# Kernel optimization log

Hardware: AMD Instinct MI355X
Metric: run time of the kernel (lower is better)

Reference implementation:

```python
import jax, jax.numpy as jnp
import numpy as np

N, E, IN, HID, EE, L, NB = 20000, 256000, 64, 128, 32, 3, 8


def _silu(x):
    return x * jax.nn.sigmoid(x)


def setup_inputs() -> dict:
    key = jax.random.key(0)
    ks = list(jax.random.split(key, 32))

    def nrm(k, shape, fan_in):
        return jax.random.normal(k, shape, dtype=jnp.float32) / np.sqrt(fan_in)

    inp = {}
    inp["H_t"] = jax.random.normal(ks[0], (N, IN), dtype=jnp.float32)
    inp["X_t"] = jax.random.normal(ks[1], (N, 3), dtype=jnp.float32)
    inp["cond_embedding"] = jax.random.normal(ks[2], (N, HID), dtype=jnp.float32)
    inp["t"] = jax.random.uniform(ks[3], (N,), dtype=jnp.float32)
    inp["edges"] = jax.random.randint(ks[4], (2, E), 0, N)
    inp["edge_types"] = jax.random.randint(ks[5], (E,), 0, 2)
    inp["generate_mask"] = jax.random.bernoulli(ks[6], 0.7, (N,))
    inp["batch_ids"] = jnp.sort(jax.random.randint(ks[7], (N,), 0, NB))
    # input MLP: (IN + 2*HID) -> HID -> HID -> HID, 3 linear layers
    d0 = IN + 2 * HID
    inp["mlp_W0"] = nrm(ks[8], (d0, HID), d0)
    inp["mlp_b0"] = jnp.zeros((HID,), jnp.float32)
    inp["mlp_W1"] = nrm(ks[9], (HID, HID), HID)
    inp["mlp_b1"] = jnp.zeros((HID,), jnp.float32)
    inp["mlp_W2"] = nrm(ks[10], (HID, HID), HID)
    inp["mlp_b2"] = jnp.zeros((HID,), jnp.float32)
    inp["edge_table"] = jax.random.normal(ks[11], (2, EE), dtype=jnp.float32)
    # encoder (EGNN-style message passing), stacked over L layers
    de = 2 * HID + 1 + EE  # [h_src, h_dst, dist^2, edge_embed]
    inp["We"] = nrm(ks[12], (L, de, HID), de)
    inp["be"] = jnp.zeros((L, HID), jnp.float32)
    inp["Wx"] = nrm(ks[13], (L, HID, 1), HID)
    inp["bx"] = jnp.zeros((L, 1), jnp.float32)
    inp["Wh"] = nrm(ks[14], (L, 2 * HID, HID), 2 * HID)
    inp["bh"] = jnp.zeros((L, HID), jnp.float32)
    inp["h2i_W"] = nrm(ks[15], (HID, IN), HID)
    inp["h2i_b"] = jnp.zeros((IN,), jnp.float32)
    return inp


def reference(H_t, X_t, cond_embedding, t, mlp_W0, mlp_b0, mlp_W1, mlp_b1,
              mlp_W2, mlp_b2, edge_table, We, be, Wx, bx, Wh, bh,
              h2i_W, h2i_b, edges, edge_types, generate_mask, batch_ids):
    n = H_t.shape[0]
    hid = mlp_W2.shape[1]
    # sinusoidal time embedding (dim = hidden_size)
    half = hid // 2
    freqs = jnp.exp(jnp.arange(half, dtype=jnp.float32) * (-np.log(10000.0) / (half - 1)))
    ang = t[:, None] * freqs[None, :]
    t_embed = jnp.concatenate([jnp.sin(ang), jnp.cos(ang)], axis=-1)  # (N, hid)
    # input MLP
    feat = jnp.concatenate([H_t, cond_embedding, t_embed], axis=-1)
    h = jax.nn.relu(feat @ mlp_W0 + mlp_b0)
    h = jax.nn.relu(h @ mlp_W1 + mlp_b1)
    h = h @ mlp_W2 + mlp_b2
    eemb = edge_table[edge_types]  # (E, EE)
    src, dst = edges[0], edges[1]
    cnt = jax.ops.segment_sum(jnp.ones((src.shape[0], 1), h.dtype), dst, num_segments=n)
    x = X_t
    for l in range(We.shape[0]):
        diff = x[src] - x[dst]                              # (E, 3)
        d2 = jnp.sum(diff * diff, axis=-1, keepdims=True)   # (E, 1)
        m_in = jnp.concatenate([h[src], h[dst], d2, eemb], axis=-1)
        msg = _silu(m_in @ We[l] + be[l])                   # (E, hid)
        w = msg @ Wx[l] + bx[l]                             # (E, 1)
        agg_x = jax.ops.segment_sum(diff * w, dst, num_segments=n)
        x = x + agg_x / (cnt + 1.0)
        agg_m = jax.ops.segment_sum(msg, dst, num_segments=n)
        h = h + _silu(jnp.concatenate([h, agg_m], axis=-1) @ Wh[l] + bh[l])
    mask = generate_mask[:, None]
    v_X = jnp.where(mask, x, jnp.zeros_like(x))
    v_H = jnp.where(mask, h @ h2i_W + h2i_b, 0.0)
    return (v_H, v_X)
```

## Files before the change

### kernel.cpp

```cpp
#include <hip/hip_runtime.h>
#include <math.h>

#define NN 20000
#define NE 256000
#define IN_DIM 64
#define HID 128
#define DE 289
#define D0 320
#define TILE_E 64
#define NB64 313
#define NUB 8
#define SRCMASK 0x3FFFFFFF

typedef unsigned short u16;
typedef unsigned int u32;
typedef unsigned long long u64;
typedef __attribute__((ext_vector_type(8))) short short8;
typedef __attribute__((ext_vector_type(4))) float float4v;

#define OFF_WE   0
#define OFF_W0   122880
#define OFF_W1   163840
#define OFF_W2   180224
#define OFF_WH   196608
#define OFF_H2I  294912
#define PACK_TOT 303104

static __device__ __forceinline__ u16 f2bf(float f) {
    unsigned int u = __float_as_uint(f);
    u += 0x7fffu + ((u >> 16) & 1u);
    return (u16)(u >> 16);
}
static __device__ __forceinline__ float bf2f(u16 s) {
    return __uint_as_float(((unsigned int)s) << 16);
}
static __device__ __forceinline__ float bflo(u32 u) { return bf2f((u16)(u & 0xffffu)); }
static __device__ __forceinline__ float bfhi(u32 u) { return bf2f((u16)(u >> 16)); }
static __device__ __forceinline__ u32 pack2(float a, float b) {
    return (u32)f2bf(a) | ((u32)f2bf(b) << 16);
}
static __device__ __forceinline__ uint4 pack8(const float* v) {
    uint4 r;
    r.x = (u32)f2bf(v[0]) | ((u32)f2bf(v[1]) << 16);
    r.y = (u32)f2bf(v[2]) | ((u32)f2bf(v[3]) << 16);
    r.z = (u32)f2bf(v[4]) | ((u32)f2bf(v[5]) << 16);
    r.w = (u32)f2bf(v[6]) | ((u32)f2bf(v[7]) << 16);
    return r;
}
static __device__ __forceinline__ float silu(float v) {
    return v * (1.f / (1.f + __expf(-v)));
}

__global__ __launch_bounds__(256) void hist_kernel(
    const float* __restrict__ X_t, const int* __restrict__ edges,
    float* __restrict__ x, int* __restrict__ deg)
{
    int gid = blockIdx.x * blockDim.x + threadIdx.x;
    int stride = gridDim.x * blockDim.x;
    for (int i = gid; i < NN * 3; i += stride) x[i] = X_t[i];
    for (int e = gid; e < NE; e += stride)
        atomicAdd(&deg[edges[NE + e]], 1);
}

__global__ __launch_bounds__(1024) void scan_kernel(
    const int* __restrict__ deg, int* __restrict__ row_start, int* __restrict__ head)
{
    __shared__ int s[1024];
    int tx = threadIdx.x;
    const int per = (NN + 1023) / 1024;
    int st = tx * per, en = st + per;
    if (st > NN) st = NN;
    if (en > NN) en = NN;
    int sum = 0;
    for (int i = st; i < en; ++i) sum += deg[i];
    s[tx] = sum;
    __syncthreads();
    for (int off = 1; off < 1024; off <<= 1) {
        int t = (tx >= off) ? s[tx - off] : 0;
        __syncthreads();
        s[tx] += t;
        __syncthreads();
    }
    int run = (tx == 0) ? 0 : s[tx - 1];
    for (int i = st; i < en; ++i) {
        row_start[i] = run; head[i] = run; run += deg[i];
    }
    if (tx == 1023) row_start[NN] = run;
}

__global__ __launch_bounds__(256) void scatter_kernel(
    const int* __restrict__ edges, const int* __restrict__ etype,
    int* __restrict__ head,
    int* __restrict__ src_s)
{
    int gid = blockIdx.x * blockDim.x + threadIdx.x;
    int stride = gridDim.x * blockDim.x;
    for (int e = gid; e < NE; e += stride) {
        int d = edges[NE + e];
        int p = atomicAdd(&head[d], 1);
        src_s[p] = edges[e] | (etype[e] << 30);
    }
}

__global__ __launch_bounds__(256) void pack_all_kernel(
    const float* __restrict__ We, const float* __restrict__ W0,
    const float* __restrict__ W1, const float* __restrict__ W2,
    const float* __restrict__ Wh, const float* __restrict__ h2i,
    u16* __restrict__ Bp)
{
    int idx = blockIdx.x * 256 + threadIdx.x;
    if (idx >= PACK_TOT) return;
    const float* src; int N = 128, Ksrc; int r;
    if (idx < OFF_W0) {
        int layer = idx / 40960; r = idx - layer * 40960;
        src = We + (size_t)layer * DE * HID; Ksrc = DE;
    } else if (idx < OFF_W1) { r = idx - OFF_W0; src = W0; Ksrc = 320; }
    else if (idx < OFF_W2)   { r = idx - OFF_W1; src = W1; Ksrc = 128; }
    else if (idx < OFF_WH)   { r = idx - OFF_W2; src = W2; Ksrc = 128; }
    else if (idx < OFF_H2I) {
        int t = idx - OFF_WH; int layer = t / 32768; r = t - layer * 32768;
        src = Wh + (size_t)layer * 256 * HID; Ksrc = 256;
    } else { r = idx - OFF_H2I; src = h2i; Ksrc = 128; N = 64; }
    int ntc = N / 16;
    int j = r & 7, lane = (r >> 3) & 63;
    int rem = r >> 9;
    int nt = rem % ntc, ks = rem / ntc;
    int k = ks * 32 + ((lane >> 4) << 3) + j;
    int c = nt * 16 + (lane & 15);
    Bp[idx] = f2bf((k < Ksrc) ? src[(size_t)k * N + c] : 0.f);
}

__global__ __launch_bounds__(256) void precomp_tv_kernel(
    const float* __restrict__ edge_table, const float* __restrict__ We,
    const float* __restrict__ be, float* __restrict__ tv, float* __restrict__ wed2)
{
    int idx = blockIdx.x * 256 + threadIdx.x;
    if (idx < 768) {
        int f = idx & 127, t = (idx >> 7) & 1, l = idx >> 8;
        float acc = be[l * 128 + f];
        const float* W = We + (size_t)l * DE * HID;
        #pragma unroll
        for (int k = 0; k < 32; ++k)
            acc += edge_table[t * 32 + k] * W[(size_t)(257 + k) * HID + f];
        tv[l * 256 + t * 128 + f] = acc;
    } else if (idx < 1152) {
        int r = idx - 768;
        int f = r & 127, l = r >> 7;
        wed2[l * 128 + f] = We[(size_t)l * DE * HID + (size_t)256 * HID + f];
    }
}

__global__ __launch_bounds__(256) void node_mlp_mfma_kernel(
    const float* __restrict__ H_t, const float* __restrict__ cond,
    const float* __restrict__ t_in,
    const u16* __restrict__ W0p, const float* __restrict__ b0,
    const u16* __restrict__ W1p, const float* __restrict__ b1,
    const u16* __restrict__ W2p, const float* __restrict__ b2,
    const u16* __restrict__ WEp, u16* __restrict__ Cbf,
    float* __restrict__ h, u16* __restrict__ h_bf)
{
    __shared__ u16 s_A[64 * 64];
    __shared__ u16 s_B[64 * 128];
    __shared__ u16 s_h[64 * 128];
    __shared__ float s_t[64];

    int tx = threadIdx.x;
    int n0 = blockIdx.x * 64;
    int l = tx & 63, w = tx >> 6;
    int mt_base = (w & 1) * 2, nt_base = (w >> 1) * 4;
    const float cfr = -logf(10000.f) / 63.f;

    if (tx < 64) s_t[tx] = (n0 + tx < NN) ? t_in[n0 + tx] : 0.f;

    float4v acc[2][4];
    #pragma unroll
    for (int mi = 0; mi < 2; ++mi)
        #pragma unroll
        for (int ni = 0; ni < 4; ++ni) acc[mi][ni] = (float4v){0.f,0.f,0.f,0.f};

    for (int t = 0; t < 5; ++t) {
        __syncthreads();
        #pragma unroll
        for (int it = 0; it < 2; ++it) {
            int flat = it * 256 + tx;
            int n = flat >> 3, sl = flat & 7;
            int c = sl ^ (n & 7);
            int k0 = t * 64 + c * 8;
            float tv8[8];
            int gn = n0 + n;
            if (gn < NN) {
                if (k0 < 192) {
                    const float* src = (k0 < 64) ? &H_t[(size_t)gn * IN_DIM + k0]
                                                 : &cond[(size_t)gn * HID + (k0 - 64)];
                    float4 a = *(const float4*)src;
                    float4 b = *(const float4*)(src + 4);
                    tv8[0]=a.x; tv8[1]=a.y; tv8[2]=a.z; tv8[3]=a.w;
                    tv8[4]=b.x; tv8[5]=b.y; tv8[6]=b.z; tv8[7]=b.w;
                } else {
                    float tv = s_t[n];
                    int jj = (k0 - 192) & 63;
                    bool is_sin = (k0 < 256);
                    #pragma unroll
                    for (int jx = 0; jx < 8; ++jx) {
                        float ang = tv * __expf(cfr * (float)(jj + jx));
                        tv8[jx] = is_sin ? __sinf(ang) : __cosf(ang);
                    }
                }
            } else {
                #pragma unroll
                for (int jx = 0; jx < 8; ++jx) tv8[jx] = 0.f;
            }
            *(uint4*)&s_A[n * 64 + sl * 8] = pack8(tv8);
        }
        #pragma unroll
        for (int it = 0; it < 4; ++it) {
            int flat = it * 256 + tx;
            ((uint4*)s_B)[flat] = ((const uint4*)(W0p + (size_t)t * 8192))[flat];
        }
        __syncthreads();
        #pragma unroll
        for (int s = 0; s < 2; ++s) {
            short8 af[2], bfv[4];
            #pragma unroll
            for (int mi = 0; mi < 2; ++mi) {
                int m = (mt_base + mi) * 16 + (l & 15);
                int c = s * 4 + (l >> 4);
                int slot = c ^ (l & 7);
                af[mi] = *(const short8*)(s_A + m * 64 + slot * 8);
            }
            #pragma unroll
            for (int ni = 0; ni < 4; ++ni)
                bfv[ni] = *(const short8*)(s_B + ((s * 8 + nt_base + ni) * 64 + l) * 8);
            #pragma unroll
            for (int mi = 0; mi < 2; ++mi)
                #pragma unroll
                for (int ni = 0; ni < 4; ++ni)
                    acc[mi][ni] = __builtin_amdgcn_mfma_f32_16x16x32_bf16(
                        af[mi], bfv[ni], acc[mi][ni], 0, 0, 0);
        }
    }
    #pragma unroll
    for (int mi = 0; mi < 2; ++mi) {
        #pragma unroll
        for (int ni = 0; ni < 4; ++ni) {
            int f = (nt_base + ni) * 16 + (l & 15);
            float bv = b0[f];
            #pragma unroll
            for (int r = 0; r < 4; ++r) {
                int m = (mt_base + mi) * 16 + (l >> 4) * 4 + r;
                float v = fmaxf(acc[mi][ni][r] + bv, 0.f);
                int slot = (f >> 3) ^ (m & 7);
                s_h[m * 128 + slot * 8 + (f & 7)] = f2bf(v);
            }
            acc[mi][ni] = (float4v){0.f,0.f,0.f,0.f};
        }
    }
    for (int t = 0; t < 2; ++t) {
        __syncthreads();
        #pragma unroll
        for (int it = 0; it < 4; ++it) {
            int flat = it * 256 + tx;
            ((uint4*)s_B)[flat] = ((const uint4*)(W1p + (size_t)t * 8192))[flat];
        }
        __syncthreads();
        #pragma unroll
        for (int s = 0; s < 2; ++s) {
            short8 af[2], bfv[4];
            #pragma unroll
            for (int mi = 0; mi < 2; ++mi) {
                int m = (mt_base + mi) * 16 + (l & 15);
                int c = t * 8 + s * 4 + (l >> 4);
                int slot = c ^ (l & 7);
                af[mi] = *(const short8*)(s_h + m * 128 + slot * 8);
            }
            #pragma unroll
            for (int ni = 0; ni < 4; ++ni)
                bfv[ni] = *(const short8*)(s_B + ((s * 8 + nt_base + ni) * 64 + l) * 8);
            #pragma unroll
            for (int mi = 0; mi < 2; ++mi)
                #pragma unroll
                for (int ni = 0; ni < 4; ++ni)
                    acc[mi][ni] = __builtin_amdgcn_mfma_f32_16x16x32_bf16(
                        af[mi], bfv[ni], acc[mi][ni], 0, 0, 0);
        }
    }
    __syncthreads();
    #pragma unroll
// ... 23 lines not shown
        #pragma unroll
        for (int s = 0; s < 2; ++s) {
            short8 af[2], bfv[4];
            #pragma unroll
            for (int mi = 0; mi < 2; ++mi) {
                int m = (mt_base + mi) * 16 + (l & 15);
                int c = t * 8 + s * 4 + (l >> 4);
                int slot = c ^ (l & 7);
                af[mi] = *(const short8*)(s_h + m * 128 + slot * 8);
            }
            #pragma unroll
            for (int ni = 0; ni < 4; ++ni)
                bfv[ni] = *(const short8*)(s_B + ((s * 8 + nt_base + ni) * 64 + l) * 8);
            #pragma unroll
            for (int mi = 0; mi < 2; ++mi)
                #pragma unroll
                for (int ni = 0; ni < 4; ++ni)
                    acc[mi][ni] = __builtin_amdgcn_mfma_f32_16x16x32_bf16(
                        af[mi], bfv[ni], acc[mi][ni], 0, 0, 0);
        }
    }
    __syncthreads();
    #pragma unroll
    for (int mi = 0; mi < 2; ++mi) {
        #pragma unroll
        for (int ni = 0; ni < 4; ++ni) {
            int f = (nt_base + ni) * 16 + (l & 15);
            float bv = b2[f];
            #pragma unroll
            for (int r = 0; r < 4; ++r) {
                int m = (mt_base + mi) * 16 + (l >> 4) * 4 + r;
                int gn = n0 + m;
                float v = acc[mi][ni][r] + bv;
                int slot = (f >> 3) ^ (m & 7);
                s_h[m * 128 + slot * 8 + (f & 7)] = f2bf(v);
                if (gn < NN) {
                    h[(size_t)gn * HID + f] = v;
                    h_bf[(size_t)gn * HID + f] = f2bf(v);
                }
            }
        }
    }

    for (int sd = 0; sd < 2; ++sd) {
        #pragma unroll
        for (int mi = 0; mi < 2; ++mi)
            #pragma unroll
            for (int ni = 0; ni < 4; ++ni) acc[mi][ni] = (float4v){0.f,0.f,0.f,0.f};
        #pragma unroll
        for (int th = 0; th < 2; ++th) {
            int t = sd * 2 + th;
            __syncthreads();
            #pragma unroll
            for (int it = 0; it < 4; ++it) {
                int flat = it * 256 + tx;
                ((uint4*)s_B)[flat] = ((const uint4*)(WEp + (size_t)t * 8192))[flat];
            }
            __syncthreads();
            #pragma unroll
            for (int s = 0; s < 2; ++s) {
                short8 af[2], bfv[4];
                #pragma unroll
                for (int mi = 0; mi < 2; ++mi) {
                    int m = (mt_base + mi) * 16 + (l & 15);
                    int c = th * 8 + s * 4 + (l >> 4);
                    int slot = c ^ (l & 7);
                    af[mi] = *(const short8*)(s_h + m * 128 + slot * 8);
                }
                #pragma unroll
                for (int ni = 0; ni < 4; ++ni)
                    bfv[ni] = *(const short8*)(s_B + ((s * 8 + nt_base + ni) * 64 + l) * 8);
                #pragma unroll
                for (int mi = 0; mi < 2; ++mi)
                    #pragma unroll
                    for (int ni = 0; ni < 4; ++ni)
                        acc[mi][ni] = __builtin_amdgcn_mfma_f32_16x16x32_bf16(
                            af[mi], bfv[ni], acc[mi][ni], 0, 0, 0);
            }
        }
        #pragma unroll
        for (int mi = 0; mi < 2; ++mi) {
            #pragma unroll
            for (int ni = 0; ni < 4; ++ni) {
                int f = sd * 128 + (nt_base + ni) * 16 + (l & 15);
                #pragma unroll
                for (int r = 0; r < 4; ++r) {
                    int m = (mt_base + mi) * 16 + (l >> 4) * 4 + r;
                    int gn = n0 + m;
                    if (gn < NN)
                        Cbf[(size_t)gn * 256 + f] = f2bf(acc[mi][ni][r]);
                }
            }
        }
    }
}

__global__ __launch_bounds__(256) void cvec_kernel(
    const u16* __restrict__ h_bf, const u16* __restrict__ WEp,
    u16* __restrict__ Cbf)
{
    __shared__ u16 s_A[64 * 64];
    __shared__ u16 s_B[64 * 128];

    int tx = threadIdx.x;
    int n0 = blockIdx.x * 64;
    int l = tx & 63, w = tx >> 6;
    int mt_base = (w & 1) * 2, nt_base = (w >> 1) * 4;

    float4v acc[2][2][4];
    #pragma unroll
    for (int sd = 0; sd < 2; ++sd)
        #pragma unroll
        for (int mi = 0; mi < 2; ++mi)
            #pragma unroll
            for (int ni = 0; ni < 4; ++ni)
                acc[sd][mi][ni] = (float4v){0.f,0.f,0.f,0.f};

    for (int t = 0; t < 4; ++t) {
        __syncthreads();
        #pragma unroll
        for (int it = 0; it < 2; ++it) {
            int flat = it * 256 + tx;
            int n = flat >> 3, sl = flat & 7;
            int c = sl ^ (n & 7);
            int gn = n0 + n;
            uint4 v = make_uint4(0,0,0,0);
            if (gn < NN) v = *(const uint4*)(h_bf + (size_t)gn * 128 + (t & 1) * 64 + c * 8);
            *(uint4*)&s_A[n * 64 + sl * 8] = v;
        }
        #pragma unroll
        for (int it = 0; it < 4; ++it) {
            int flat = it * 256 + tx;
            ((uint4*)s_B)[flat] = ((const uint4*)(WEp + (size_t)t * 8192))[flat];
        }
        __syncthreads();
        int sd = t >> 1;
        #pragma unroll
        for (int s = 0; s < 2; ++s) {
            short8 af[2], bfv[4];
            #pragma unroll
            for (int mi = 0; mi < 2; ++mi) {
                int m = (mt_base + mi) * 16 + (l & 15);
                int c = s * 4 + (l >> 4);
                int slot = c ^ (l & 7);
                af[mi] = *(const short8*)(s_A + m * 64 + slot * 8);
            }
            #pragma unroll
            for (int ni = 0; ni < 4; ++ni)
                bfv[ni] = *(const short8*)(s_B + ((s * 8 + nt_base + ni) * 64 + l) * 8);
            #pragma unroll
            for (int mi = 0; mi < 2; ++mi)
                #pragma unroll
                for (int ni = 0; ni < 4; ++ni)
                    acc[sd][mi][ni] = __builtin_amdgcn_mfma_f32_16x16x32_bf16(
                        af[mi], bfv[ni], acc[sd][mi][ni], 0, 0, 0);
        }
    }
    #pragma unroll
    for (int sd = 0; sd < 2; ++sd) {
        #pragma unroll
        for (int mi = 0; mi < 2; ++mi) {
            #pragma unroll
            for (int ni = 0; ni < 4; ++ni) {
                int f = sd * 128 + (nt_base + ni) * 16 + (l & 15);
                #pragma unroll
                for (int r = 0; r < 4; ++r) {
                    int m = (mt_base + mi) * 16 + (l >> 4) * 4 + r;
                    int gn = n0 + m;
                    if (gn < NN)
                        Cbf[(size_t)gn * 256 + f] = f2bf(acc[sd][mi][ni][r]);
                }
            }
        }
    }
}

__global__ __launch_bounds__(512, 4) void node_fused_kernel(
    float* __restrict__ h, u16* __restrict__ h_bf,
    const float* __restrict__ x_in, float* __restrict__ x_out,
    const u16* __restrict__ Cbf,
    const int* __restrict__ src_s,
    const int* __restrict__ row_start,
    const float* __restrict__ tv_l, const float* __restrict__ wed2_l,
    const float* __restrict__ Wx_l, const float* __restrict__ bx_l,
    const u16* __restrict__ Whp_l, const float* __restrict__ bh_l)
{
    __shared__ u16 s_A[16 * 256];

    int tx = threadIdx.x;
    int n0 = blockIdx.x * NUB;
    int l = tx & 63, w = tx >> 6;
    int i = w;
    int gn = n0 + i;
    int p = l & 31, q = l >> 5;

    if (tx < 256) {
        int n = tx >> 4, c = tx & 15;
        int slot = c ^ (n & 7);
        uint4 v = make_uint4(0, 0, 0, 0);
        if (n < NUB) v = *(const uint4*)(h_bf + (size_t)(n0 + n) * 128 + c * 8);
        *(uint4*)&s_A[n * 256 + slot * 8] = v;
    } else if (tx < 384) {
        int n = 8 + ((tx - 256) >> 4), c = 16 + (tx & 15);
        int slot = c ^ (n & 7);
        *(uint4*)&s_A[n * 256 + slot * 8] = make_uint4(0, 0, 0, 0);
    }

    float c0[4], d01[4], wed[4], wx[4];
    {
        uint2 cd = *(const uint2*)(Cbf + (size_t)gn * 256 + 128 + p * 4);
        float cdv0 = bflo(cd.x), cdv1 = bfhi(cd.x), cdv2 = bflo(cd.y), cdv3 = bfhi(cd.y);
        float4 t0 = *(const float4*)(tv_l + p * 4);
        float4 t1 = *(const float4*)(tv_l + 128 + p * 4);
        float4 wd = *(const float4*)(wed2_l + p * 4);
        float4 wv = *(const float4*)(Wx_l + p * 4);
        c0[0] = t0.x + cdv0; c0[1] = t0.y + cdv1; c0[2] = t0.z + cdv2; c0[3] = t0.w + cdv3;
        d01[0] = t1.x - t0.x; d01[1] = t1.y - t0.y; d01[2] = t1.z - t0.z; d01[3] = t1.w - t0.w;
        wed[0] = wd.x; wed[1] = wd.y; wed[2] = wd.z; wed[3] = wd.w;
        wx[0] = wv.x; wx[1] = wv.y; wx[2] = wv.z; wx[3] = wv.w;
    }
    float bx32 = bx_l[0] * (1.f / 32.f);

    int rs = row_start[gn], re = row_start[gn + 1];
    int d = re - rs;

    float xd0 = x_in[gn * 3 + 0], xd1 = x_in[gn * 3 + 1], xd2 = x_in[gn * 3 + 2];

    float ag[4] = {0.f, 0.f, 0.f, 0.f};
    float sx = 0.f, sy = 0.f, sz = 0.f;

    for (int e0 = 0; e0 < d; e0 += 64) {
        int nchunk = d - e0; if (nchunk > 64) nchunk = 64;
        int sp_l = (l < nchunk) ? src_s[rs + e0 + l] : 0;
        float gx_l = 0.f, gy_l = 0.f, gz_l = 0.f, d2_l = 0.f;
        if (l < nchunk) {
            int sm = sp_l & SRCMASK;
            gx_l = x_in[sm * 3 + 0] - xd0;
            gy_l = x_in[sm * 3 + 1] - xd1;
            gz_l = x_in[sm * 3 + 2] - xd2;
            d2_l = gx_l * gx_l + gy_l * gy_l + gz_l * gz_l;
        }

        auto FETCH = [&](int lj, uint2& cc, float& et) {
            int spE = __shfl(sp_l, lj);
            cc = make_uint2(0u, 0u); et = 0.f;
            if (lj < nchunk) {
                cc = *(const uint2*)(Cbf + (size_t)(spE & SRCMASK) * 256 + p * 4);
                et = (float)((u32)spE >> 30);
            }
        };
        auto PROC = [&](int lj, uint2 cc, float ee) {
            float dxe = __shfl(gx_l, lj);
            float dye = __shfl(gy_l, lj);
            float dze = __shfl(gz_l, lj);
            float d2e = __shfl(d2_l, lj);
            float av[4];
            av[0] = bflo(cc.x); av[1] = bfhi(cc.x);
            av[2] = bflo(cc.y); av[3] = bfhi(cc.y);
            float wpart = bx32;
            #pragma unroll
            for (int f = 0; f < 4; ++f) {
                float t = __fmaf_rn(d2e, wed[f], c0[f]);
                t = __fmaf_rn(ee, d01[f], t);
                float v = av[f] + t;
                float m = silu(v);
                ag[f] += m;
                wpart = __fmaf_rn(m, wx[f], wpart);
            }
            sx = __fmaf_rn(dxe, wpart, sx);
            sy = __fmaf_rn(dye, wpart, sy);
            sz = __fmaf_rn(dze, wpart, sz);
        };

        int ljA = q, ljB = q + 2, ljC = q + 4, ljD = q + 6, ljn = q + 8;
        uint2 ccA, ccB, ccC, ccD; float etA, etB, etC, etD;
        FETCH(ljA, ccA, etA); FETCH(ljB, ccB, etB);
        FETCH(ljC, ccC, etC); FETCH(ljD, ccD, etD);
        while (ljA < nchunk) {
            PROC(ljA, ccA, etA); ljA = ljn; ljn += 2; FETCH(ljA, ccA, etA);
            if (ljB >= nchunk) break;
            PROC(ljB, ccB, etB); ljB = ljn; ljn += 2; FETCH(ljB, ccB, etB);
            if (ljC >= nchunk) break;
            PROC(ljC, ccC, etC); ljC = ljn; ljn += 2; FETCH(ljC, ccC, etC);
            if (ljD >= nchunk) break;
            PROC(ljD, ccD, etD); ljD = ljn; ljn += 2; FETCH(ljD, ccD, etD);
        }
    }

    #pragma unroll
    for (int f = 0; f < 4; ++f) ag[f] += __shfl_xor(ag[f], 32);
    #pragma unroll
    for (int off = 1; off <= 32; off <<= 1) {
        sx += __shfl_xor(sx, off);
        sy += __shfl_xor(sy, off);
        sz += __shfl_xor(sz, off);
    }
    if (l < 32) {
        int c2 = 16 + (p >> 1);
        int slot = c2 ^ (i & 7);
        uint2 o;
        o.x = pack2(ag[0], ag[1]);
        o.y = pack2(ag[2], ag[3]);
        *(uint2*)&s_A[i * 256 + slot * 8 + (p & 1) * 4] = o;
    }
    if (l == 0) {
        float inv = 1.f / ((float)d + 1.f);
        x_out[gn * 3 + 0] = xd0 + sx * inv;
        x_out[gn * 3 + 1] = xd1 + sy * inv;
        x_out[gn * 3 + 2] = xd2 + sz * inv;
    }

    __syncthreads();

    float4v acc = (float4v){0.f, 0.f, 0.f, 0.f};
    #pragma unroll
    for (int t = 0; t < 4; ++t) {
        #pragma unroll
        for (int s = 0; s < 2; ++s) {
            int m = l & 15;
            int c = t * 8 + s * 4 + (l >> 4);
            int slot = c ^ (l & 7);
            short8 af = *(const short8*)(s_A + m * 256 + slot * 8);
            short8 bfv = *(const short8*)(Whp_l + (size_t)t * 8192 + ((s * 8 + w) * 64 + l) * 8);
            acc = __builtin_amdgcn_mfma_f32_16x16x32_bf16(af, bfv, acc, 0, 0, 0);
        }
    }
    {
        int f = w * 16 + (l & 15);
        float bv = bh_l[f];
        #pragma unroll
        for (int r = 0; r < 4; ++r) {
            int m = (l >> 4) * 4 + r;
            if (m < NUB) {
                int gn2 = n0 + m;
                float v = acc[r] + bv;
                float hn = h[(size_t)gn2 * HID + f] + silu(v);
                h[(size_t)gn2 * HID + f] = hn;
                h_bf[(size_t)gn2 * HID + f] = f2bf(hn);
            }
        }
    }
}

__global__ __launch_bounds__(256) void final_mfma_kernel(
    const u16* __restrict__ h_bf, const float* __restrict__ x,
    const int* __restrict__ gmask,
    const u16* __restrict__ h2ip, const float* __restrict__ b,
    float* __restrict__ out)
{
    __shared__ u16 s_A[64 * 128];
    __shared__ u16 s_B[4096];

    int tx = threadIdx.x;
    int n0 = blockIdx.x * 64;
    int l = tx & 63, w = tx >> 6;
    int mt_base = (w & 1) * 2, nt_base = (w >> 1) * 2;

    #pragma unroll
    for (int it = 0; it < 4; ++it) {
        int flat = it * 256 + tx;
        int n = flat >> 4, c = flat & 15;
        int slot = c ^ (n & 7);
        int gn = n0 + n;
        uint4 v = make_uint4(0,0,0,0);
        if (gn < NN) v = *(const uint4*)(h_bf + (size_t)gn * 128 + c * 8);
        *(uint4*)&s_A[n * 128 + slot * 8] = v;
    }

    float4v acc[2][2];
    #pragma unroll
    for (int mi = 0; mi < 2; ++mi)
        #pragma unroll
        for (int ni = 0; ni < 2; ++ni) acc[mi][ni] = (float4v){0.f,0.f,0.f,0.f};

    for (int t = 0; t < 2; ++t) {
        __syncthreads();
        #pragma unroll
        for (int it = 0; it < 2; ++it) {
            int flat = it * 256 + tx;
            ((uint4*)s_B)[flat] = ((const uint4*)(h2ip + (size_t)t * 4096))[flat];
        }
        __syncthreads();
        #pragma unroll
        for (int s = 0; s < 2; ++s) {
            short8 af[2], bfv[2];
            #pragma unroll
            for (int mi = 0; mi < 2; ++mi) {
                int m = (mt_base + mi) * 16 + (l & 15);
                int c = t * 8 + s * 4 + (l >> 4);
                int slot = c ^ (l & 7);
                af[mi] = *(const short8*)(s_A + m * 128 + slot * 8);
            }
            #pragma unroll
            for (int ni = 0; ni < 2; ++ni)
                bfv[ni] = *(const short8*)(s_B + ((s * 4 + nt_base + ni) * 64 + l) * 8);
            #pragma unroll
            for (int mi = 0; mi < 2; ++mi)
                #pragma unroll
                for (int ni = 0; ni < 2; ++ni)
                    acc[mi][ni] = __builtin_amdgcn_mfma_f32_16x16x32_bf16(
                        af[mi], bfv[ni], acc[mi][ni], 0, 0, 0);
        }
    }
    #pragma unroll
    for (int mi = 0; mi < 2; ++mi) {
        #pragma unroll
        for (int ni = 0; ni < 2; ++ni) {
            int f = (nt_base + ni) * 16 + (l & 15);
            float bv = b[f];
            #pragma unroll
            for (int r = 0; r < 4; ++r) {
                int m = (mt_base + mi) * 16 + (l >> 4) * 4 + r;
                int gn = n0 + m;
                if (gn < NN)
                    out[(size_t)gn * IN_DIM + f] = gmask[gn] ? (acc[mi][ni][r] + bv) : 0.f;
            }
        }
    }
    if (tx < 192) {
        int i = tx / 3, c = tx % 3;
        int gn = n0 + i;
// ... 255 lines not shown
        acc[4] += f1.x*w; acc[5] += f1.y*w; acc[6] += f1.z*w; acc[7] += f1.w*w;
        acc[8] += f2.x*w; acc[9] += f2.y*w; acc[10]+= f2.z*w; acc[11]+= f2.w*w;
        acc[12]+= f3.x*w; acc[13]+= f3.y*w; acc[14]+= f3.z*w; acc[15]+= f3.w*w;
    }
    #pragma unroll
    for (int i = 0; i < 16; ++i) {
        float v = acc[i];
        h[(n0 + i) * HID + tx] = s_in[tx][i] + silu(v);
    }
    if (tx < 48) {
        int i = tx / 3, c = tx % 3;
        int n = n0 + i;
        x[n * 3 + c] += agg_x[n * 3 + c] / (cnt[n] + 1.f);
    }
}

__global__ __launch_bounds__(64) void final_fb_kernel(
    const float* __restrict__ h, const float* __restrict__ x,
    const int* __restrict__ gmask,
    const float* __restrict__ W, const float* __restrict__ b,
    float* __restrict__ out)
{
    __shared__ float s_h[8][HID];
    int n0 = blockIdx.x * 8;
    int tx = threadIdx.x;
    for (int idx = tx; idx < 8 * HID; idx += 64) {
        int i = idx >> 7, k = idx & 127;
        s_h[i][k] = h[(n0 + i) * HID + k];
    }
    __syncthreads();
    float acc[8];
    float bv = b[tx];
    #pragma unroll
    for (int i = 0; i < 8; ++i) acc[i] = bv;
    for (int k = 0; k < HID; ++k) {
        float w = W[k * IN_DIM + tx];
        #pragma unroll
        for (int i = 0; i < 8; ++i) acc[i] += s_h[i][k] * w;
    }
    #pragma unroll
    for (int i = 0; i < 8; ++i) {
        int n = n0 + i;
        out[n * IN_DIM + tx] = gmask[n] ? acc[i] : 0.f;
    }
    if (tx < 24) {
        int i = tx / 3, c = tx % 3;
        int n = n0 + i;
        out[NN * IN_DIM + n * 3 + c] = gmask[n] ? x[n * 3 + c] : 0.f;
    }
}

extern "C" void kernel_launch(void* const* d_in, const int* in_sizes, int n_in,
                              void* d_out, int out_size, void* d_ws, size_t ws_size,
                              hipStream_t stream) {
    const float* H_t   = (const float*)d_in[0];
    const float* X_t   = (const float*)d_in[1];
    const float* cond  = (const float*)d_in[2];
    const float* t_in  = (const float*)d_in[3];
    const int*   edges = (const int*)d_in[4];
    const int*   etype = (const int*)d_in[5];
    const int*   gmask = (const int*)d_in[6];
    const float* W0 = (const float*)d_in[8];
    const float* b0 = (const float*)d_in[9];
    const float* W1 = (const float*)d_in[10];
    const float* b1 = (const float*)d_in[11];
    const float* W2 = (const float*)d_in[12];
    const float* b2 = (const float*)d_in[13];
    const float* edge_table = (const float*)d_in[14];
    const float* We = (const float*)d_in[15];
    const float* be = (const float*)d_in[16];
    const float* Wx = (const float*)d_in[17];
    const float* bx = (const float*)d_in[18];
    const float* Wh = (const float*)d_in[19];
    const float* bh = (const float*)d_in[20];
    const float* h2i_W = (const float*)d_in[21];
    const float* h2i_b = (const float*)d_in[22];

    char* p = (char*)d_ws;
    float* h = (float*)p;           p += (size_t)NN * HID * 4;
    u16* h_bf = (u16*)p;            p += (size_t)NN * HID * 2;
    float* xa = (float*)p;          p += (size_t)NN * 3 * 4;
    float* xb = (float*)p;          p += (size_t)NN * 3 * 4;
    u16* Cbf = (u16*)p;             p += (size_t)NN * 256 * 2;
    u16* Bpack = (u16*)p;           p += (size_t)PACK_TOT * 2;
    float* tv = (float*)p;          p += (size_t)768 * 4;
    float* wed2 = (float*)p;        p += (size_t)384 * 4;
    int* row_start = (int*)p;       p += (size_t)(NN + 4) * 4;
    int* deg = (int*)p;             p += (size_t)NN * 4;
    int* head = (int*)p;            p += (size_t)NN * 4;
    int* src_s = (int*)p;           p += (size_t)NE * 4;
    size_t need = (size_t)(p - (char*)d_ws);

    if (ws_size >= need) {
        hipMemsetAsync(deg, 0, NN * sizeof(int), stream);
        hist_kernel<<<256, 256, 0, stream>>>(X_t, edges, xa, deg);
        scan_kernel<<<1, 1024, 0, stream>>>(deg, row_start, head);
        scatter_kernel<<<256, 256, 0, stream>>>(edges, etype, head, src_s);
        pack_all_kernel<<<(PACK_TOT + 255) / 256, 256, 0, stream>>>(
            We, W0, W1, W2, Wh, h2i_W, Bpack);
        precomp_tv_kernel<<<5, 256, 0, stream>>>(edge_table, We, be, tv, wed2);
        node_mlp_mfma_kernel<<<NB64, 256, 0, stream>>>(
            H_t, cond, t_in,
            Bpack + OFF_W0, b0, Bpack + OFF_W1, b1, Bpack + OFF_W2, b2,
            Bpack + OFF_WE, Cbf,
            h, h_bf);
        for (int l = 0; l < 3; ++l) {
            if (l > 0)
                cvec_kernel<<<NB64, 256, 0, stream>>>(
                    h_bf, Bpack + OFF_WE + (size_t)l * 40960, Cbf);
            const float* xin = (l & 1) ? xb : xa;
            float* xout = (l & 1) ? xa : xb;
            node_fused_kernel<<<NN / NUB, 512, 0, stream>>>(
                h, h_bf, xin, xout, Cbf, src_s, row_start,
                tv + (size_t)l * 256, wed2 + (size_t)l * 128,
                Wx + l * HID, bx + l,
                Bpack + OFF_WH + (size_t)l * 32768, bh + l * HID);
        }
        final_mfma_kernel<<<NB64, 256, 0, stream>>>(
            h_bf, xb, gmask, Bpack + OFF_H2I, h2i_b, (float*)d_out);
    } else {
        float* ws    = (float*)d_ws;
        float* fh    = ws;
        float* fx    = fh + NN * HID;
        float* cnt   = fx + NN * 3;
        float* fagg_m = cnt + NN;
        float* fagg_x = fagg_m + NN * HID;

        hipMemsetAsync(cnt, 0, NN * sizeof(float), stream);
        init_fb_kernel<<<256, 256, 0, stream>>>(X_t, edges, fx, cnt);
        node_mlp_kernel<<<NN / 16, 128, 0, stream>>>(H_t, cond, t_in,
                                                     W0, b0, W1, b1, W2, b2, fh);
        for (int l = 0; l < 3; ++l) {
            hipMemsetAsync(fagg_m, 0, (size_t)NN * 131 * sizeof(float), stream);
            edge_gemm_fb_kernel<<<NE / TILE_E, 256, 0, stream>>>(
                fh, fx, edges, etype, edge_table,
                We + (size_t)l * DE * HID, be + l * HID,
                Wx + l * HID, bx + l, fagg_m, fagg_x);
            node_update_fb_kernel<<<NN / 16, 128, 0, stream>>>(
                fh, fx, fagg_m, fagg_x, cnt,
                Wh + (size_t)l * 256 * HID, bh + l * HID);
        }
        final_fb_kernel<<<NN / 8, 64, 0, stream>>>(fh, fx, gmask, h2i_W, h2i_b, (float*)d_out);
    }
}
```

Measured before the change: 372.0 us.

## Split edge aggregation from Wh update and fuse next-layer cvec into Wh kernel

Replaces the per-node fused kernel, where each wave handled one node's edges plus a tiny MFMA, with two kernels. The first is a wave-per-4-nodes edge aggregation kernel that walks a contiguous CSR edge range using readlane broadcasts and writes bf16 agg_m. The second is a 64-node-tile MFMA kernel that applies the Wh update and immediately computes the next layer's per-node We projections from shared memory, which removes the separate cvec launch. The edge-type constant is also folded into Cbf at write time. This trades an extra agg_bf round trip through global memory for better MFMA tiling and fewer launches, and the per-wave serial flush logic may cost latency.

```diff
diff --git a/kernel.cpp b/kernel.cpp
--- a/kernel.cpp
+++ b/kernel.cpp
@@ -9,7 +9,7 @@
 #define D0 320
 #define TILE_E 64
 #define NB64 313
-#define NUB 8
+#define NPW 4
 #define SRCMASK 0x3FFFFFFF
 
 typedef unsigned short u16;
@@ -49,6 +49,9 @@
 }
 static __device__ __forceinline__ float silu(float v) {
     return v * (1.f / (1.f + __expf(-v)));
+}
+static __device__ __forceinline__ float rdlane_f(float v, int j) {
+    return __int_as_float(__builtin_amdgcn_readlane(__float_as_int(v), j));
 }
 
 __global__ __launch_bounds__(256) void hist_kernel(
@@ -156,7 +159,8 @@
     const u16* __restrict__ W0p, const float* __restrict__ b0,
     const u16* __restrict__ W1p, const float* __restrict__ b1,
     const u16* __restrict__ W2p, const float* __restrict__ b2,
-    const u16* __restrict__ WEp, u16* __restrict__ Cbf,
+    const u16* __restrict__ WEp, const float* __restrict__ tv0,
+    u16* __restrict__ Cbf,
     float* __restrict__ h, u16* __restrict__ h_bf)
 {
     __shared__ u16 s_A[64 * 64];
@@ -197,12 +201,12 @@
                     tv8[0]=a.x; tv8[1]=a.y; tv8[2]=a.z; tv8[3]=a.w;
                     tv8[4]=b.x; tv8[5]=b.y; tv8[6]=b.z; tv8[7]=b.w;
                 } else {
-                    float tv = s_t[n];
+                    float tvv = s_t[n];
                     int jj = (k0 - 192) & 63;
                     bool is_sin = (k0 < 256);
                     #pragma unroll
                     for (int jx = 0; jx < 8; ++jx) {
-                        float ang = tv * __expf(cfr * (float)(jj + jx));
+                        float ang = tvv * __expf(cfr * (float)(jj + jx));
                         tv8[jx] = is_sin ? __sinf(ang) : __cosf(ang);
                     }
                 }
@@ -392,59 +396,182 @@
         for (int mi = 0; mi < 2; ++mi) {
             #pragma unroll
             for (int ni = 0; ni < 4; ++ni) {
-                int f = sd * 128 + (nt_base + ni) * 16 + (l & 15);
+                int fq = (nt_base + ni) * 16 + (l & 15);
+                int f = sd * 128 + fq;
+                float tadd = (sd == 1) ? tv0[fq] : 0.f;
                 #pragma unroll
                 for (int r = 0; r < 4; ++r) {
                     int m = (mt_base + mi) * 16 + (l >> 4) * 4 + r;
                     int gn = n0 + m;
                     if (gn < NN)
-                        Cbf[(size_t)gn * 256 + f] = f2bf(acc[mi][ni][r]);
+                        Cbf[(size_t)gn * 256 + f] = f2bf(acc[mi][ni][r] + tadd);
                 }
             }
         }
     }
 }
 
-__global__ __launch_bounds__(256) void cvec_kernel(
-    const u16* __restrict__ h_bf, const u16* __restrict__ WEp,
-    u16* __restrict__ Cbf)
+__global__ __launch_bounds__(256) void edge_agg_kernel(
+    const float* __restrict__ x_in, float* __restrict__ x_out,
+    const u16* __restrict__ Cbf, u16* __restrict__ agg_bf,
+    const int* __restrict__ src_s,
+    const int* __restrict__ row_start,
+    const float* __restrict__ tv_l, const float* __restrict__ wed2_l,
+    const float* __restrict__ Wx_l, const float* __restrict__ bx_l)
+{
+    int tx = threadIdx.x;
+    int l = tx & 63;
+    int wg = blockIdx.x * 4 + (tx >> 6);
+    int n0w = wg * NPW;
+
+    float2 wed = *(const float2*)(wed2_l + 2 * l);
+    float2 wxv = *(const float2*)(Wx_l + 2 * l);
+    float tva0 = tv_l[2 * l],       tva1 = tv_l[2 * l + 1];
+    float tvb0 = tv_l[128 + 2 * l], tvb1 = tv_l[128 + 2 * l + 1];
+    float d01_0 = tvb0 - tva0, d01_1 = tvb1 - tva1;
+    float bx64 = bx_l[0] * (1.f / 64.f);
+
+    int rsv = row_start[n0w + (l < NPW ? l : NPW)];
+    int rs0w = __builtin_amdgcn_readlane(rsv, 0);
+    int reN  = __builtin_amdgcn_readlane(rsv, NPW);
+    int b1 = __builtin_amdgcn_readlane(rsv, 1);
+    int b2 = __builtin_amdgcn_readlane(rsv, 2);
+    int b3 = __builtin_amdgcn_readlane(rsv, 3);
+
+    u32 cdA = *(const u32*)(Cbf + (size_t)(n0w + 0) * 256 + 128 + 2 * l);
+    u32 cdB = *(const u32*)(Cbf + (size_t)(n0w + 1) * 256 + 128 + 2 * l);
+    u32 cdC = *(const u32*)(Cbf + (size_t)(n0w + 2) * 256 + 128 + 2 * l);
+    u32 cdD = *(const u32*)(Cbf + (size_t)(n0w + 3) * 256 + 128 + 2 * l);
+
+    int cur = 0;
+    int nstart = rs0w;
+    int bnext = b1;
+    float c0f0 = bflo(cdA), c0f1 = bfhi(cdA);
+    float ag0 = 0.f, ag1 = 0.f, sx = 0.f, sy = 0.f, sz = 0.f;
+
+    auto FLUSH = [&]() {
+        float rx = sx, ry = sy, rz = sz;
+        #pragma unroll
+        for (int off = 1; off < 64; off <<= 1) {
+            rx += __shfl_xor(rx, off);
+            ry += __shfl_xor(ry, off);
+            rz += __shfl_xor(rz, off);
+        }
+        int gn = n0w + cur;
+        *(u32*)(agg_bf + (size_t)gn * 128 + 2 * l) = pack2(ag0, ag1);
+        if (l == 0) {
+            float inv = 1.f / ((float)(bnext - nstart) + 1.f);
+            x_out[gn * 3 + 0] = x_in[gn * 3 + 0] + rx * inv;
+            x_out[gn * 3 + 1] = x_in[gn * 3 + 1] + ry * inv;
+            x_out[gn * 3 + 2] = x_in[gn * 3 + 2] + rz * inv;
+        }
+        ag0 = 0.f; ag1 = 0.f; sx = 0.f; sy = 0.f; sz = 0.f;
+        nstart = bnext;
+        cur++;
+        cdA = cdB; cdB = cdC; cdC = cdD;
+        c0f0 = bflo(cdA); c0f1 = bfhi(cdA);
+        if (cur < NPW) bnext = __builtin_amdgcn_readlane(rsv, cur + 1);
+    };
+
+    const char* cb = (const char*)Cbf;
+    int lx4 = l << 2;
+
+    for (int base = rs0w; base < reN; base += 64) {
+        int nch = reN - base; if (nch > 64) nch = 64;
+        int voff_l = 0;
+        float et_l = 0.f, gx_l = 0.f, gy_l = 0.f, gz_l = 0.f, d2_l = 0.f;
+        if (l < nch) {
+            int pos_l = base + l;
+            int sp = src_s[pos_l];
+            int sm = sp & SRCMASK;
+            int k = (pos_l >= b1) + (pos_l >= b2) + (pos_l >= b3);
+            int dn = n0w + k;
+            voff_l = sm * 512;
+            et_l = (float)((u32)sp >> 30);
+            gx_l = x_in[sm * 3 + 0] - x_in[dn * 3 + 0];
+            gy_l = x_in[sm * 3 + 1] - x_in[dn * 3 + 1];
+            gz_l = x_in[sm * 3 + 2] - x_in[dn * 3 + 2];
+            d2_l = gx_l * gx_l + gy_l * gy_l + gz_l * gz_l;
+        }
+        auto LD = [&](int t) -> u32 {
+            int so = __builtin_amdgcn_readlane(voff_l, t & 63);
+            return *(const u32*)(cb + (u32)so + lx4);
+        };
+        auto BODY = [&](int j, u32 cc) {
+            int pos = base + j;
+            while (pos == bnext) FLUSH();
+            float s_et = rdlane_f(et_l, j);
+            float s_dx = rdlane_f(gx_l, j);
+            float s_dy = rdlane_f(gy_l, j);
+            float s_dz = rdlane_f(gz_l, j);
+            float s_d2 = rdlane_f(d2_l, j);
+            float av0 = bflo(cc), av1 = bfhi(cc);
+            float t0 = __fmaf_rn(s_d2, wed.x, c0f0);
+            t0 = __fmaf_rn(s_et, d01_0, t0) + av0;
+            float t1 = __fmaf_rn(s_d2, wed.y, c0f1);
+            t1 = __fmaf_rn(s_et, d01_1, t1) + av1;
+            float m0 = silu(t0), m1 = silu(t1);
+            ag0 += m0; ag1 += m1;
+            float wpart = __fmaf_rn(m1, wxv.y, __fmaf_rn(m0, wxv.x, bx64));
+            sx = __fmaf_rn(s_dx, wpart, sx);
+            sy = __fmaf_rn(s_dy, wpart, sy);
+            sz = __fmaf_rn(s_dz, wpart, sz);
+        };
+
+        u32 cA = LD(0), cB = LD(1), cC = LD(2), cD = LD(3);
+        int j = 0;
+        while (j < nch) {
+            BODY(j, cA); cA = LD(j + 4); if (++j >= nch) break;
+            BODY(j, cB); cB = LD(j + 4); if (++j >= nch) break;
+            BODY(j, cC); cC = LD(j + 4); if (++j >= nch) break;
+            BODY(j, cD); cD = LD(j + 4); ++j;
+        }
+    }
+    while (cur < NPW) FLUSH();
+}
+
+__global__ __launch_bounds__(256) void wh_cvec_kernel(
+    float* __restrict__ h, u16* __restrict__ h_bf,
+    const u16* __restrict__ agg_bf,
+    const u16* __restrict__ Whp_l, const float* __restrict__ bh_l,
+    const u16* __restrict__ WEp_next, const float* __restrict__ tv_next,
+    u16* __restrict__ Cbf, int do_cvec)
 {
     __shared__ u16 s_A[64 * 64];
     __shared__ u16 s_B[64 * 128];
+    __shared__ u16 s_h[64 * 128];
 
     int tx = threadIdx.x;
     int n0 = blockIdx.x * 64;
     int l = tx & 63, w = tx >> 6;
     int mt_base = (w & 1) * 2, nt_base = (w >> 1) * 4;
 
-    float4v acc[2][2][4];
-    #pragma unroll
-    for (int sd = 0; sd < 2; ++sd)
-        #pragma unroll
-        for (int mi = 0; mi < 2; ++mi)
-            #pragma unroll
-            for (int ni = 0; ni < 4; ++ni)
-                acc[sd][mi][ni] = (float4v){0.f,0.f,0.f,0.f};
+    float4v acc[2][4];
+    #pragma unroll
+    for (int mi = 0; mi < 2; ++mi)
+        #pragma unroll
+        for (int ni = 0; ni < 4; ++ni) acc[mi][ni] = (float4v){0.f,0.f,0.f,0.f};
 
     for (int t = 0; t < 4; ++t) {
         __syncthreads();
+        const u16* Asrc = (t < 2) ? h_bf : agg_bf;
+        int koff = (t & 1) * 64;
         #pragma unroll
         for (int it = 0; it < 2; ++it) {
             int flat = it * 256 + tx;
             int n = flat >> 3, sl = flat & 7;
             int c = sl ^ (n & 7);
             int gn = n0 + n;
-            uint4 v = make_uint4(0,0,0,0);
-            if (gn < NN) v = *(const uint4*)(h_bf + (size_t)gn * 128 + (t & 1) * 64 + c * 8);
+            uint4 v = make_uint4(0, 0, 0, 0);
+            if (gn < NN) v = *(const uint4*)(Asrc + (size_t)gn * 128 + koff + c * 8);
             *(uint4*)&s_A[n * 64 + sl * 8] = v;
         }
         #pragma unroll
         for (int it = 0; it < 4; ++it) {
             int flat = it * 256 + tx;
-            ((uint4*)s_B)[flat] = ((const uint4*)(WEp + (size_t)t * 8192))[flat];
-        }
-        __syncthreads();
-        int sd = t >> 1;
+            ((uint4*)s_B)[flat] = ((const uint4*)(Whp_l + (size_t)t * 8192))[flat];
+        }
+        __syncthreads();
         #pragma unroll
         for (int s = 0; s < 2; ++s) {
             short8 af[2], bfv[4];
@@ -462,191 +589,87 @@
             for (int mi = 0; mi < 2; ++mi)
                 #pragma unroll
                 for (int ni = 0; ni < 4; ++ni)
-                    acc[sd][mi][ni] = __builtin_amdgcn_mfma_f32_16x16x32_bf16(
-                        af[mi], bfv[ni], acc[sd][mi][ni], 0, 0, 0);
-        }
-    }
-    #pragma unroll
+                    acc[mi][ni] = __builtin_amdgcn_mfma_f32_16x16x32_bf16(
+                        af[mi], bfv[ni], acc[mi][ni], 0, 0, 0);
+        }
+    }
+    __syncthreads();
+    #pragma unroll
+    for (int mi = 0; mi < 2; ++mi) {
+        #pragma unroll
+        for (int ni = 0; ni < 4; ++ni) {
+            int f = (nt_base + ni) * 16 + (l & 15);
+            float bv = bh_l[f];
+            #pragma unroll
+            for (int r = 0; r < 4; ++r) {
+                int m = (mt_base + mi) * 16 + (l >> 4) * 4 + r;
+                int gn = n0 + m;
+                float v = acc[mi][ni][r] + bv;
+                float hold = (gn < NN) ? h[(size_t)gn * HID + f] : 0.f;
+                float hn = hold + silu(v);
+                int slot = (f >> 3) ^ (m & 7);
+                s_h[m * 128 + slot * 8 + (f & 7)] = f2bf(hn);
+                if (gn < NN) {
+                    h[(size_t)gn * HID + f] = hn;
+                    h_bf[(size_t)gn * HID + f] = f2bf(hn);
+                }
+            }
+            acc[mi][ni] = (float4v){0.f,0.f,0.f,0.f};
+        }
+    }
+    if (!do_cvec) return;
     for (int sd = 0; sd < 2; ++sd) {
+        if (sd == 1) {
+            #pragma unroll
+            for (int mi = 0; mi < 2; ++mi)
+                #pragma unroll
+                for (int ni = 0; ni < 4; ++ni) acc[mi][ni] = (float4v){0.f,0.f,0.f,0.f};
+        }
+        #pragma unroll
+        for (int th = 0; th < 2; ++th) {
+            int t = sd * 2 + th;
+            __syncthreads();
+            #pragma unroll
+            for (int it = 0; it < 4; ++it) {
+                int flat = it * 256 + tx;
+                ((uint4*)s_B)[flat] = ((const uint4*)(WEp_next + (size_t)t * 8192))[flat];
+            }
+            __syncthreads();
+            #pragma unroll
+            for (int s = 0; s < 2; ++s) {
+                short8 af[2], bfv[4];
+                #pragma unroll
+                for (int mi = 0; mi < 2; ++mi) {
+                    int m = (mt_base + mi) * 16 + (l & 15);
+                    int c = th * 8 + s * 4 + (l >> 4);
+                    int slot = c ^ (l & 7);
+                    af[mi] = *(const short8*)(s_h + m * 128 + slot * 8);
+                }
+                #pragma unroll
+                for (int ni = 0; ni < 4; ++ni)
+                    bfv[ni] = *(const short8*)(s_B + ((s * 8 + nt_base + ni) * 64 + l) * 8);
+                #pragma unroll
+                for (int mi = 0; mi < 2; ++mi)
+                    #pragma unroll
+                    for (int ni = 0; ni < 4; ++ni)
+                        acc[mi][ni] = __builtin_amdgcn_mfma_f32_16x16x32_bf16(
+                            af[mi], bfv[ni], acc[mi][ni], 0, 0, 0);
+            }
+        }
         #pragma unroll
         for (int mi = 0; mi < 2; ++mi) {
             #pragma unroll
             for (int ni = 0; ni < 4; ++ni) {
-                int f = sd * 128 + (nt_base + ni) * 16 + (l & 15);
+                int fq = (nt_base + ni) * 16 + (l & 15);
+                int f = sd * 128 + fq;
+                float tadd = (sd == 1) ? tv_next[fq] : 0.f;
                 #pragma unroll
                 for (int r = 0; r < 4; ++r) {
                     int m = (mt_base + mi) * 16 + (l >> 4) * 4 + r;
                     int gn = n0 + m;
                     if (gn < NN)
-                        Cbf[(size_t)gn * 256 + f] = f2bf(acc[sd][mi][ni][r]);
+                        Cbf[(size_t)gn * 256 + f] = f2bf(acc[mi][ni][r] + tadd);
                 }
-            }
-        }
-    }
-}
-
-__global__ __launch_bounds__(512, 4) void node_fused_kernel(
-    float* __restrict__ h, u16* __restrict__ h_bf,
-    const float* __restrict__ x_in, float* __restrict__ x_out,
-    const u16* __restrict__ Cbf,
-    const int* __restrict__ src_s,
-    const int* __restrict__ row_start,
-    const float* __restrict__ tv_l, const float* __restrict__ wed2_l,
-    const float* __restrict__ Wx_l, const float* __restrict__ bx_l,
-    const u16* __restrict__ Whp_l, const float* __restrict__ bh_l)
-{
-    __shared__ u16 s_A[16 * 256];
-
-    int tx = threadIdx.x;
-    int n0 = blockIdx.x * NUB;
-    int l = tx & 63, w = tx >> 6;
-    int i = w;
-    int gn = n0 + i;
-    int p = l & 31, q = l >> 5;
-
-    if (tx < 256) {
-        int n = tx >> 4, c = tx & 15;
-        int slot = c ^ (n & 7);
-        uint4 v = make_uint4(0, 0, 0, 0);
-        if (n < NUB) v = *(const uint4*)(h_bf + (size_t)(n0 + n) * 128 + c * 8);
-        *(uint4*)&s_A[n * 256 + slot * 8] = v;
-    } else if (tx < 384) {
-        int n = 8 + ((tx - 256) >> 4), c = 16 + (tx & 15);
-        int slot = c ^ (n & 7);
-        *(uint4*)&s_A[n * 256 + slot * 8] = make_uint4(0, 0, 0, 0);
-    }
-
-    float c0[4], d01[4], wed[4], wx[4];
-    {
-        uint2 cd = *(const uint2*)(Cbf + (size_t)gn * 256 + 128 + p * 4);
-        float cdv0 = bflo(cd.x), cdv1 = bfhi(cd.x), cdv2 = bflo(cd.y), cdv3 = bfhi(cd.y);
-        float4 t0 = *(const float4*)(tv_l + p * 4);
-        float4 t1 = *(const float4*)(tv_l + 128 + p * 4);
-        float4 wd = *(const float4*)(wed2_l + p * 4);
-        float4 wv = *(const float4*)(Wx_l + p * 4);
-        c0[0] = t0.x + cdv0; c0[1] = t0.y + cdv1; c0[2] = t0.z + cdv2; c0[3] = t0.w + cdv3;
-        d01[0] = t1.x - t0.x; d01[1] = t1.y - t0.y; d01[2] = t1.z - t0.z; d01[3] = t1.w - t0.w;
-        wed[0] = wd.x; wed[1] = wd.y; wed[2] = wd.z; wed[3] = wd.w;
-        wx[0] = wv.x; wx[1] = wv.y; wx[2] = wv.z; wx[3] = wv.w;
-    }
-    float bx32 = bx_l[0] * (1.f / 32.f);
-
-    int rs = row_start[gn], re = row_start[gn + 1];
-    int d = re - rs;
-
-    float xd0 = x_in[gn * 3 + 0], xd1 = x_in[gn * 3 + 1], xd2 = x_in[gn * 3 + 2];
-
-    float ag[4] = {0.f, 0.f, 0.f, 0.f};
-    float sx = 0.f, sy = 0.f, sz = 0.f;
-
-    for (int e0 = 0; e0 < d; e0 += 64) {
-        int nchunk = d - e0; if (nchunk > 64) nchunk = 64;
-        int sp_l = (l < nchunk) ? src_s[rs + e0 + l] : 0;
-        float gx_l = 0.f, gy_l = 0.f, gz_l = 0.f, d2_l = 0.f;
-        if (l < nchunk) {
-            int sm = sp_l & SRCMASK;
-            gx_l = x_in[sm * 3 + 0] - xd0;
-            gy_l = x_in[sm * 3 + 1] - xd1;
-            gz_l = x_in[sm * 3 + 2] - xd2;
-            d2_l = gx_l * gx_l + gy_l * gy_l + gz_l * gz_l;
-        }
-
-        auto FETCH = [&](int lj, uint2& cc, float& et) {
-            int spE = __shfl(sp_l, lj);
-            cc = make_uint2(0u, 0u); et = 0.f;
-            if (lj < nchunk) {
-                cc = *(const uint2*)(Cbf + (size_t)(spE & SRCMASK) * 256 + p * 4);
-                et = (float)((u32)spE >> 30);
-            }
-        };
-        auto PROC = [&](int lj, uint2 cc, float ee) {
-            float dxe = __shfl(gx_l, lj);
-            float dye = __shfl(gy_l, lj);
-            float dze = __shfl(gz_l, lj);
-            float d2e = __shfl(d2_l, lj);
-            float av[4];
-            av[0] = bflo(cc.x); av[1] = bfhi(cc.x);
-            av[2] = bflo(cc.y); av[3] = bfhi(cc.y);
-            float wpart = bx32;
-            #pragma unroll
-            for (int f = 0; f < 4; ++f) {
-                float t = __fmaf_rn(d2e, wed[f], c0[f]);
-                t = __fmaf_rn(ee, d01[f], t);
-                float v = av[f] + t;
-                float m = silu(v);
-                ag[f] += m;
-                wpart = __fmaf_rn(m, wx[f], wpart);
-            }
-            sx = __fmaf_rn(dxe, wpart, sx);
-            sy = __fmaf_rn(dye, wpart, sy);
-            sz = __fmaf_rn(dze, wpart, sz);
-        };
-
-        int ljA = q, ljB = q + 2, ljC = q + 4, ljD = q + 6, ljn = q + 8;
-        uint2 ccA, ccB, ccC, ccD; float etA, etB, etC, etD;
-        FETCH(ljA, ccA, etA); FETCH(ljB, ccB, etB);
-        FETCH(ljC, ccC, etC); FETCH(ljD, ccD, etD);
-        while (ljA < nchunk) {
-            PROC(ljA, ccA, etA); ljA = ljn; ljn += 2; FETCH(ljA, ccA, etA);
-            if (ljB >= nchunk) break;
-            PROC(ljB, ccB, etB); ljB = ljn; ljn += 2; FETCH(ljB, ccB, etB);
-            if (ljC >= nchunk) break;
-            PROC(ljC, ccC, etC); ljC = ljn; ljn += 2; FETCH(ljC, ccC, etC);
-            if (ljD >= nchunk) break;
-            PROC(ljD, ccD, etD); ljD = ljn; ljn += 2; FETCH(ljD, ccD, etD);
-        }
-    }
-
-    #pragma unroll
-    for (int f = 0; f < 4; ++f) ag[f] += __shfl_xor(ag[f], 32);
-    #pragma unroll
-    for (int off = 1; off <= 32; off <<= 1) {
-        sx += __shfl_xor(sx, off);
-        sy += __shfl_xor(sy, off);
-        sz += __shfl_xor(sz, off);
-    }
-    if (l < 32) {
-        int c2 = 16 + (p >> 1);
-        int slot = c2 ^ (i & 7);
-        uint2 o;
-        o.x = pack2(ag[0], ag[1]);
-        o.y = pack2(ag[2], ag[3]);
-        *(uint2*)&s_A[i * 256 + slot * 8 + (p & 1) * 4] = o;
-    }
-    if (l == 0) {
-        float inv = 1.f / ((float)d + 1.f);
-        x_out[gn * 3 + 0] = xd0 + sx * inv;
-        x_out[gn * 3 + 1] = xd1 + sy * inv;
-        x_out[gn * 3 + 2] = xd2 + sz * inv;
-    }
-
-    __syncthreads();
-
-    float4v acc = (float4v){0.f, 0.f, 0.f, 0.f};
-    #pragma unroll
-    for (int t = 0; t < 4; ++t) {
-        #pragma unroll
-        for (int s = 0; s < 2; ++s) {
-            int m = l & 15;
-            int c = t * 8 + s * 4 + (l >> 4);
-            int slot = c ^ (l & 7);
-            short8 af = *(const short8*)(s_A + m * 256 + slot * 8);
-            short8 bfv = *(const short8*)(Whp_l + (size_t)t * 8192 + ((s * 8 + w) * 64 + l) * 8);
-            acc = __builtin_amdgcn_mfma_f32_16x16x32_bf16(af, bfv, acc, 0, 0, 0);
-        }
-    }
-    {
-        int f = w * 16 + (l & 15);
-        float bv = bh_l[f];
-        #pragma unroll
-        for (int r = 0; r < 4; ++r) {
-            int m = (l >> 4) * 4 + r;
-            if (m < NUB) {
-                int gn2 = n0 + m;
-                float v = acc[r] + bv;
-                float hn = h[(size_t)gn2 * HID + f] + silu(v);
-                h[(size_t)gn2 * HID + f] = hn;
-                h_bf[(size_t)gn2 * HID + f] = f2bf(hn);
             }
         }
     }
@@ -1068,6 +1091,7 @@
     float* xa = (float*)p;          p += (size_t)NN * 3 * 4;
     float* xb = (float*)p;          p += (size_t)NN * 3 * 4;
     u16* Cbf = (u16*)p;             p += (size_t)NN * 256 * 2;
+    u16* agg_bf = (u16*)p;          p += (size_t)NN * HID * 2;
     u16* Bpack = (u16*)p;           p += (size_t)PACK_TOT * 2;
     float* tv = (float*)p;          p += (size_t)768 * 4;
     float* wed2 = (float*)p;        p += (size_t)384 * 4;
@@ -1088,19 +1112,22 @@
         node_mlp_mfma_kernel<<<NB64, 256, 0, stream>>>(
             H_t, cond, t_in,
             Bpack + OFF_W0, b0, Bpack + OFF_W1, b1, Bpack + OFF_W2, b2,
-            Bpack + OFF_WE, Cbf,
+            Bpack + OFF_WE, tv, Cbf,
             h, h_bf);
         for (int l = 0; l < 3; ++l) {
-            if (l > 0)
-                cvec_kernel<<<NB64, 256, 0, stream>>>(
-                    h_bf, Bpack + OFF_WE + (size_t)l * 40960, Cbf);
             const float* xin = (l & 1) ? xb : xa;
             float* xout = (l & 1) ? xa : xb;
-            node_fused_kernel<<<NN / NUB, 512, 0, stream>>>(
-                h, h_bf, xin, xout, Cbf, src_s, row_start,
+            edge_agg_kernel<<<NN / NPW / 4, 256, 0, stream>>>(
+                xin, xout, Cbf, agg_bf, src_s, row_start,
                 tv + (size_t)l * 256, wed2 + (size_t)l * 128,
-                Wx + l * HID, bx + l,
-                Bpack + OFF_WH + (size_t)l * 32768, bh + l * HID);
+                Wx + l * HID, bx + l);
+            int do_cvec = (l < 2) ? 1 : 0;
+            wh_cvec_kernel<<<NB64, 256, 0, stream>>>(
+                h, h_bf, agg_bf,
+                Bpack + OFF_WH + (size_t)l * 32768, bh + l * HID,
+                Bpack + OFF_WE + (size_t)(do_cvec ? (l + 1) : 0) * 40960,
+                tv + (size_t)(do_cvec ? (l + 1) : 0) * 256,
+                Cbf, do_cvec);
         }
         final_mfma_kernel<<<NB64, 256, 0, stream>>>(
             h_bf, xb, gmask, Bpack + OFF_H2I, h2i_b, (float*)d_out);
```

Result: slower. 399.3 us (+7.3%).
